# Performance work log

Hardware: AMD Instinct MI355X
Metric: run time of the kernel (lower is better)

Reference implementation:

```python
import jax, jax.numpy as jnp
import numpy as np

B, T, C, H = 2, 2048, 1024, 16
D = C // H  # head dim = 64

def setup_inputs() -> dict:
    key = jax.random.key(0)
    ks = jax.random.split(key, 5)
    s = 0.02
    return {
        "x": jax.random.normal(ks[0], (B, T, C), dtype=jnp.float32),
        "Wqkv": jax.random.normal(ks[1], (C, 3 * C), dtype=jnp.float32) * s,
        "bqkv": jnp.zeros((3 * C,), dtype=jnp.float32),
        "Wproj": jax.random.normal(ks[2], (C, C), dtype=jnp.float32) * s,
        "bproj": jnp.zeros((C,), dtype=jnp.float32),
    }

def reference(x, Wqkv, bqkv, Wproj, bproj):
    b, t, c = x.shape
    qkv = x @ Wqkv + bqkv                       # [B,T,3C]
    q, k, v = jnp.split(qkv, 3, axis=-1)
    # [B,T,C] -> [B,H,T,D]
    q = q.reshape(b, t, H, D).transpose(0, 2, 1, 3)
    k = k.reshape(b, t, H, D).transpose(0, 2, 1, 3)
    v = v.reshape(b, t, H, D).transpose(0, 2, 1, 3)
    scale = 1.0 / np.sqrt(D).astype(np.float32)
    attn = jnp.einsum('bhqd,bhkd->bhqk', q, k) * scale  # [B,H,T,T]
    causal = jnp.tril(jnp.ones((t, t), dtype=bool))
    attn = jnp.where(causal, attn, jnp.float32(-jnp.inf))
    attn = jax.nn.softmax(attn, axis=-1)
    y = jnp.einsum('bhqk,bhkd->bhqd', attn, v)          # [B,H,T,D]
    y = y.transpose(0, 2, 1, 3).reshape(b, t, c)        # [B,T,C]
    return y @ Wproj + bproj
```

## Files before the change

kernel.cpp:

```cpp
#include <hip/hip_runtime.h>
#include <stdint.h>

#define B_ 2
#define T_ 2048
#define C_ 1024
#define H_ 16
#define D_ 64
#define M_ (B_*T_)
#define BHTD_ (B_*H_*T_*D_)

typedef __bf16 bf16x8 __attribute__((ext_vector_type(8)));
typedef __bf16 bf16x4 __attribute__((ext_vector_type(4)));
typedef float f32x4 __attribute__((ext_vector_type(4)));

static __device__ __forceinline__ unsigned short f32_bf16(float f) {
    unsigned int u = __float_as_uint(f);
    u += 0x7FFFu + ((u >> 16) & 1u);
    return (unsigned short)(u >> 16);
}

__global__ void cast_kernel(const float* __restrict__ in, unsigned short* __restrict__ out, int n) {
    int i = (blockIdx.x * 256 + threadIdx.x) * 4;
    if (i >= n) return;
    float4 f = *(const float4*)(in + i);
    ushort4 o;
    o.x = f32_bf16(f.x); o.y = f32_bf16(f.y); o.z = f32_bf16(f.z); o.w = f32_bf16(f.w);
    *(ushort4*)(out + i) = o;
}

__global__ void transpose_cast_kernel(const float* __restrict__ W, unsigned short* __restrict__ Wt,
                                      int K, int N) {
    __shared__ float tile[32][33];
    int n0 = blockIdx.x * 32, k0 = blockIdx.y * 32;
    int tx = threadIdx.x, ty = threadIdx.y;
    #pragma unroll
    for (int j = 0; j < 32; j += 8)
        tile[ty + j][tx] = W[(size_t)(k0 + ty + j) * N + n0 + tx];
    __syncthreads();
    #pragma unroll
    for (int j = 0; j < 32; j += 8)
        Wt[(size_t)(n0 + ty + j) * K + k0 + tx] = f32_bf16(tile[tx][ty + j]);
}

template<int EPI>
__global__ __launch_bounds__(256) void gemm_bt(
    const unsigned short* __restrict__ A,
    const unsigned short* __restrict__ Bt,
    const float* __restrict__ bias,
    unsigned short* __restrict__ out_bf16,
    float* __restrict__ out_f32,
    int M, int N, int K)
{
    __shared__ unsigned short As[2][128 * 32];
    __shared__ unsigned short Bs[2][128 * 32];
    int tid = threadIdx.x;
    int lane = tid & 63, wid = tid >> 6;
    int fr = lane & 15, fg = lane >> 4;
    int row0 = blockIdx.x * 128, col0 = blockIdx.y * 128;
    int wm = (wid >> 1) * 64, wn = (wid & 1) * 64;

    f32x4 acc[4][4];
    #pragma unroll
    for (int i = 0; i < 4; ++i)
        #pragma unroll
        for (int j = 0; j < 4; ++j)
            acc[i][j] = (f32x4){0.f, 0.f, 0.f, 0.f};

    const int srw = lane >> 2;
    const int scl = (lane & 3) * 8;
    const int c0 = wid * 2, c1 = wid * 2 + 1;

    auto stage = [&](int buf, int k0) {
        __builtin_amdgcn_global_load_lds(
            (const __attribute__((address_space(1))) void*)(A + (size_t)(row0 + c0 * 16 + srw) * K + k0 + scl),
            (__attribute__((address_space(3))) void*)(As[buf] + c0 * 512), 16, 0, 0);
        __builtin_amdgcn_global_load_lds(
            (const __attribute__((address_space(1))) void*)(A + (size_t)(row0 + c1 * 16 + srw) * K + k0 + scl),
            (__attribute__((address_space(3))) void*)(As[buf] + c1 * 512), 16, 0, 0);
        __builtin_amdgcn_global_load_lds(
            (const __attribute__((address_space(1))) void*)(Bt + (size_t)(col0 + c0 * 16 + srw) * K + k0 + scl),
            (__attribute__((address_space(3))) void*)(Bs[buf] + c0 * 512), 16, 0, 0);
        __builtin_amdgcn_global_load_lds(
            (const __attribute__((address_space(1))) void*)(Bt + (size_t)(col0 + c1 * 16 + srw) * K + k0 + scl),
            (__attribute__((address_space(3))) void*)(Bs[buf] + c1 * 512), 16, 0, 0);
    };

    stage(0, 0);
    __syncthreads();

    int cur = 0;
    for (int k0 = 0; k0 < K; k0 += 32) {
        if (k0 + 32 < K) stage(cur ^ 1, k0 + 32);

        bf16x8 af[4], bfr[4];
        #pragma unroll
        for (int i = 0; i < 4; ++i) {
            af[i]  = *(const bf16x8*)(As[cur] + (wm + i * 16 + fr) * 32 + fg * 8);
            bfr[i] = *(const bf16x8*)(Bs[cur] + (wn + i * 16 + fr) * 32 + fg * 8);
        }
        #pragma unroll
        for (int mi = 0; mi < 4; ++mi)
            #pragma unroll
            for (int ni = 0; ni < 4; ++ni)
                acc[mi][ni] = __builtin_amdgcn_mfma_f32_16x16x32_bf16(af[mi], bfr[ni], acc[mi][ni], 0, 0, 0);

        __syncthreads();
        cur ^= 1;
    }

    #pragma unroll
    for (int mi = 0; mi < 4; ++mi) {
        int rowb = row0 + wm + mi * 16 + fg * 4;
        #pragma unroll
        for (int ni = 0; ni < 4; ++ni) {
            int col = col0 + wn + ni * 16 + fr;
            float bv = bias[col];
            #pragma unroll
            for (int r = 0; r < 4; ++r) {
                float v = acc[mi][ni][r] + bv;
                int rr = rowb + r;
                if (EPI == 0) {
                    int part = col >> 10, c = col & 1023;
                    int h = c >> 6, d = c & 63;
                    int b = rr >> 11, t = rr & 2047;
                    if (part == 0) v *= 0.18033688011112042f;
                    size_t idx;
                    if (part == 2)
                        idx = (size_t)2 * BHTD_ + ((size_t)(b * H_ + h) * D_ + d) * T_ + t;
                    else
                        idx = (size_t)part * BHTD_ + ((size_t)(b * H_ + h) * T_ + t) * D_ + d;
                    out_bf16[idx] = f32_bf16(v);
                } else {
                    out_f32[(size_t)rr * N + col] = v;
                }
            }
        }
    }
}

__global__ __launch_bounds__(256) void attn_kernel(
    const unsigned short* __restrict__ qg,
    const unsigned short* __restrict__ kg,
    const unsigned short* __restrict__ vtg,
    unsigned short* __restrict__ y)
{
    const int id = blockIdx.x;
    const int xcd = id & 7, loc = id >> 3;
    const int bh = xcd * 4 + (loc & 3);
    const int iq = loc >> 2;
    const int chlo = iq, chhi = 31 - iq;
    const int b = bh >> 4, h = bh & 15;
    const int tid = threadIdx.x, wid = tid >> 6, lane = tid & 63;
    const int fr = lane & 15, fg = lane >> 4;

    const unsigned short* qp = qg + (size_t)bh * (T_ * D_);
    const unsigned short* kp = kg + (size_t)bh * (T_ * D_);
    const unsigned short* vp = vtg + (size_t)bh * (D_ * T_);

    __shared__ __align__(16) char Ks[2][64 * 128];
    __shared__ __align__(16) char Vs[2][64 * 128];
    __shared__ __align__(16) char Ps[4][32 * 128];
    char* Pw = Ps[wid];

    const int rhi = chhi * 64 + wid * 16;
    const int rlo = chlo * 64 + wid * 16;

    const int srow = tid >> 3;
    const int scb  = (tid & 7) * 16;
    const int sws  = scb ^ ((srow & 7) << 4);

    bf16x8 qhi[2], qlo[2];
    #pragma unroll
    for (int kd = 0; kd < 2; ++kd) {
        qhi[kd] = *(const bf16x8*)(qp + (size_t)(rhi + fr) * D_ + kd * 32 + fg * 8);
        qlo[kd] = *(const bf16x8*)(qp + (size_t)(rlo + fr) * D_ + kd * 32 + fg * 8);
    }

    f32x4 oHi[4], oLo[4];
    float lHi = 0.f, lLo = 0.f;
    #pragma unroll
    for (int n = 0; n < 4; ++n) {
        oHi[n] = (f32x4){0.f, 0.f, 0.f, 0.f};
        oLo[n] = (f32x4){0.f, 0.f, 0.f, 0.f};
    }

    const int ntk  = chhi + 1;
    const int ntlo = chlo + 1;

    {
        uint4 k0 = *(const uint4*)(kp + (size_t)srow        * D_ + (scb >> 1));
        uint4 k1 = *(const uint4*)(kp + (size_t)(srow + 32) * D_ + (scb >> 1));
        uint4 v0 = *(const uint4*)(vp + (size_t)srow        * T_ + (scb >> 1));
        uint4 v1 = *(const uint4*)(vp + (size_t)(srow + 32) * T_ + (scb >> 1));
        *(uint4*)(Ks[0] + srow * 128 + sws)        = k0;
        *(uint4*)(Ks[0] + (srow + 32) * 128 + sws) = k1;
        *(uint4*)(Vs[0] + srow * 128 + sws)        = v0;
        *(uint4*)(Vs[0] + (srow + 32) * 128 + sws) = v1;
    }
    __syncthreads();

    int cur = 0;
    for (int t = 0; t < ntk; ++t) {
        const int kv0 = t * 64;
        const int kv1 = (t + 1 < ntk) ? kv0 + 64 : kv0;

        uint4 pk0 = *(const uint4*)(kp + (size_t)(kv1 + srow)      * D_ + (scb >> 1));
        uint4 pk1 = *(const uint4*)(kp + (size_t)(kv1 + srow + 32) * D_ + (scb >> 1));
        uint4 pv0 = *(const uint4*)(vp + (size_t)srow        * T_ + kv1 + (scb >> 1));
        uint4 pv1 = *(const uint4*)(vp + (size_t)(srow + 32) * T_ + kv1 + (scb >> 1));

        const char* Kb = Ks[cur];
        const char* Vb = Vs[cur];
        const unsigned lsw = (unsigned)((fr & 7) << 4);
        const bool lo_act = (t < ntlo);

        f32x4 sh[4], sl[4];
        #pragma unroll
        for (int n = 0; n < 4; ++n) {
            sh[n] = (f32x4){0.f, 0.f, 0.f, 0.f};
            sl[n] = (f32x4){0.f, 0.f, 0.f, 0.f};
        }
        #pragma unroll
        for (int kd = 0; kd < 2; ++kd)
            #pragma unroll
            for (int n = 0; n < 4; ++n) {
                bf16x8 kf = *(const bf16x8*)(Kb + (n * 16 + fr) * 128 +
                                             (((unsigned)(kd * 64 + fg * 16)) ^ lsw));
                sh[n] = __builtin_amdgcn_mfma_f32_16x16x32_bf16(kf, qhi[kd], sh[n], 0, 0, 0);
                if (lo_act)
                    sl[n] = __builtin_amdgcn_mfma_f32_16x16x32_bf16(kf, qlo[kd], sl[n], 0, 0, 0);
            }

        bf16x8 vf[4][2];
        #pragma unroll
        for (int nd = 0; nd < 4; ++nd)
            #pragma unroll
            for (int kk = 0; kk < 2; ++kk)
                vf[nd][kk] = *(const bf16x8*)(Vb + (nd * 16 + fr) * 128 +
                                              (((unsigned)(kk * 64 + fg * 16)) ^ lsw));

        {
            const bool masked = (t == chhi);
            const int qrow = rhi + fr;
            const unsigned prow = (unsigned)fr * 128;
            #pragma unroll
            for (int n = 0; n < 4; ++n) {
                float x0 = sh[n][0], x1 = sh[n][1], x2 = sh[n][2], x3 = sh[n][3];
                if (masked) {
                    const int kvb = kv0 + n * 16 + fg * 4;
                    if (kvb     > qrow) x0 = -1e30f;
                    if (kvb + 1 > qrow) x1 = -1e30f;
                    if (kvb + 2 > qrow) x2 = -1e30f;
                    if (kvb + 3 > qrow) x3 = -1e30f;
                }
                const float p0 = exp2f(x0), p1 = exp2f(x1);
                const float p2 = exp2f(x2), p3 = exp2f(x3);
                lHi += (p0 + p1) + (p2 + p3);
                bf16x4 pk4 = {(__bf16)p0, (__bf16)p1, (__bf16)p2, (__bf16)p3};
                *(uint2*)(Pw + ((prow + (unsigned)(n * 32 + fg * 8)) ^ lsw)) =
                    __builtin_bit_cast(uint2, pk4);
            }
        }
        {
            const unsigned prow = (unsigned)fr * 128;
            #pragma unroll
            for (int kk = 0; kk < 2; ++kk) {
                bf16x8 pb = *(const bf16x8*)(Pw + ((prow + (unsigned)(kk * 64 + fg * 16)) ^ lsw));
                #pragma unroll
                for (int nd = 0; nd < 4; ++nd)
                    oHi[nd] = __builtin_amdgcn_mfma_f32_16x16x32_bf16(vf[nd][kk], pb, oHi[nd], 0, 0, 0);
            }
        }
        if (lo_act) {
            const bool masked = (t == chlo);
            const int qrow = rlo + fr;
            const unsigned prow = (unsigned)(16 + fr) * 128;
            #pragma unroll
            for (int n = 0; n < 4; ++n) {
                float x0 = sl[n][0], x1 = sl[n][1], x2 = sl[n][2], x3 = sl[n][3];
                if (masked) {
                    const int kvb = kv0 + n * 16 + fg * 4;
                    if (kvb     > qrow) x0 = -1e30f;
                    if (kvb + 1 > qrow) x1 = -1e30f;
                    if (kvb + 2 > qrow) x2 = -1e30f;
                    if (kvb + 3 > qrow) x3 = -1e30f;
                }
                const float p0 = exp2f(x0), p1 = exp2f(x1);
                const float p2 = exp2f(x2), p3 = exp2f(x3);
                lLo += (p0 + p1) + (p2 + p3);
                bf16x4 pk4 = {(__bf16)p0, (__bf16)p1, (__bf16)p2, (__bf16)p3};
                *(uint2*)(Pw + ((prow + (unsigned)(n * 32 + fg * 8)) ^ lsw)) =
                    __builtin_bit_cast(uint2, pk4);
            }
            const unsigned prow2 = (unsigned)(16 + fr) * 128;
            #pragma unroll
            for (int kk = 0; kk < 2; ++kk) {
                bf16x8 pb = *(const bf16x8*)(Pw + ((prow2 + (unsigned)(kk * 64 + fg * 16)) ^ lsw));
                #pragma unroll
                for (int nd = 0; nd < 4; ++nd)
                    oLo[nd] = __builtin_amdgcn_mfma_f32_16x16x32_bf16(vf[nd][kk], pb, oLo[nd], 0, 0, 0);
            }
        }

        {
            char* Kn = Ks[cur ^ 1];
            char* Vn = Vs[cur ^ 1];
            *(uint4*)(Kn + srow * 128 + sws)        = pk0;
            *(uint4*)(Kn + (srow + 32) * 128 + sws) = pk1;
            *(uint4*)(Vn + srow * 128 + sws)        = pv0;
            *(uint4*)(Vn + (srow + 32) * 128 + sws) = pv1;
        }
        __syncthreads();
        cur ^= 1;
    }

    #pragma unroll
    for (int s = 0; s < 2; ++s) {
        float rs = s ? lLo : lHi;
        rs += __shfl_xor(rs, 16);
        rs += __shfl_xor(rs, 32);
        const float inv = 1.f / rs;
        const int trow = (s ? rlo : rhi) + fr;
        f32x4* oT = s ? oLo : oHi;
        #pragma unroll
        for (int nd = 0; nd < 4; ++nd) {
            bf16x4 ov = {(__bf16)(oT[nd][0] * inv), (__bf16)(oT[nd][1] * inv),
                         (__bf16)(oT[nd][2] * inv), (__bf16)(oT[nd][3] * inv)};
            *(uint2*)(y + ((size_t)b * T_ + trow) * C_ + h * 64 + nd * 16 + fg * 4) =
                __builtin_bit_cast(uint2, ov);
        }
    }
}

extern "C" void kernel_launch(void* const* d_in, const int* in_sizes, int n_in,
                              void* d_out, int out_size, void* d_ws, size_t ws_size,
                              hipStream_t stream) {
    const float* x     = (const float*)d_in[0];
    const float* Wqkv  = (const float*)d_in[1];
    const float* bqkv  = (const float*)d_in[2];
    const float* Wproj = (const float*)d_in[3];
    const float* bproj = (const float*)d_in[4];
    float* out = (float*)d_out;

    char* ws = (char*)d_ws;
    unsigned short* x_bf    = (unsigned short*)(ws);
    unsigned short* wqkv_t  = (unsigned short*)(ws + 8388608);
    unsigned short* wproj_t = (unsigned short*)(ws + 14680064);
    unsigned short* qkv     = (unsigned short*)(ws + 16777216);
    unsigned short* ybuf    = (unsigned short*)(ws + 41943040);

    cast_kernel<<<(M_ * C_) / 4 / 256, 256, 0, stream>>>(x, x_bf, M_ * C_);
    transpose_cast_kernel<<<dim3(3072 / 32, 1024 / 32), dim3(32, 8), 0, stream>>>(Wqkv, wqkv_t, 1024, 3072);
    transpose_cast_kernel<<<dim3(1024 / 32, 1024 / 32), dim3(32, 8), 0, stream>>>(Wproj, wproj_t, 1024, 1024);

    gemm_bt<0><<<dim3(M_ / 128, 3072 / 128), 256, 0, stream>>>(
        x_bf, wqkv_t, bqkv, qkv, nullptr, M_, 3072, 1024);

    attn_kernel<<<dim3(512), 256, 0, stream>>>(
        qkv, qkv + (size_t)BHTD_, qkv + 2 * (size_t)BHTD_, ybuf);

    gemm_bt<1><<<dim3(M_ / 128, 1024 / 128), 256, 0, stream>>>(
        ybuf, wproj_t, bproj, nullptr, out, M_, 1024, 1024);
}
```

Before: 126.5 us.

## Restructure attention to 32x32 MFMA tiles with direct-to-LDS loads and register P

Rewrites the attention kernel to use 32x32x16 MFMA with 128-thread blocks (two waves, 32 query rows each) over 1024 blocks. K/V tiles are staged with global_load_lds directly into LDS instead of going through registers. The P matrix stays in registers, repacked with permlane32_swap, instead of round-tripping through LDS. Causal load balancing moves from pairing hi/lo chunks within one block to ordering blocks by chunk. The intent is to cut LDS traffic and register staging and to raise MFMA efficiency, at the risk of lower per-block reuse and more blocks to schedule.

```diff
diff --git a/kernel.cpp b/kernel.cpp
--- a/kernel.cpp
+++ b/kernel.cpp
@@ -11,12 +11,19 @@
 
 typedef __bf16 bf16x8 __attribute__((ext_vector_type(8)));
 typedef __bf16 bf16x4 __attribute__((ext_vector_type(4)));
+typedef __bf16 bf16x2 __attribute__((ext_vector_type(2)));
 typedef float f32x4 __attribute__((ext_vector_type(4)));
+typedef float f32x16 __attribute__((ext_vector_type(16)));
 
 static __device__ __forceinline__ unsigned short f32_bf16(float f) {
     unsigned int u = __float_as_uint(f);
     u += 0x7FFFu + ((u >> 16) & 1u);
     return (unsigned short)(u >> 16);
+}
+
+static __device__ __forceinline__ int pack_bf16_2(float a, float b) {
+    bf16x2 v = {(__bf16)a, (__bf16)b};
+    return __builtin_bit_cast(int, v);
 }
 
 __global__ void cast_kernel(const float* __restrict__ in, unsigned short* __restrict__ out, int n) {
@@ -138,196 +145,191 @@
     }
 }
 
-__global__ __launch_bounds__(256) void attn_kernel(
+__global__ __launch_bounds__(128) void attn_kernel(
     const unsigned short* __restrict__ qg,
     const unsigned short* __restrict__ kg,
     const unsigned short* __restrict__ vtg,
     unsigned short* __restrict__ y)
 {
     const int id = blockIdx.x;
-    const int xcd = id & 7, loc = id >> 3;
-    const int bh = xcd * 4 + (loc & 3);
-    const int iq = loc >> 2;
-    const int chlo = iq, chhi = 31 - iq;
+    const int xcd = id & 7, j = id >> 3;
+    const int c = j & 31, g = j >> 5;
+    int chunk;
+    if      (g == 0) chunk = 31 - c;
+    else if (g == 1) chunk = c;
+    else if (g == 2) chunk = (15 - c) & 31;
+    else             chunk = (c + 16) & 31;
+    const int bh = xcd * 4 + (c >> 3);
     const int b = bh >> 4, h = bh & 15;
     const int tid = threadIdx.x, wid = tid >> 6, lane = tid & 63;
-    const int fr = lane & 15, fg = lane >> 4;
+    const int lq = lane & 31, hi = lane >> 5;
 
     const unsigned short* qp = qg + (size_t)bh * (T_ * D_);
-    const unsigned short* kp = kg + (size_t)bh * (T_ * D_);
-    const unsigned short* vp = vtg + (size_t)bh * (D_ * T_);
-
-    __shared__ __align__(16) char Ks[2][64 * 128];
-    __shared__ __align__(16) char Vs[2][64 * 128];
-    __shared__ __align__(16) char Ps[4][32 * 128];
-    char* Pw = Ps[wid];
-
-    const int rhi = chhi * 64 + wid * 16;
-    const int rlo = chlo * 64 + wid * 16;
-
-    const int srow = tid >> 3;
-    const int scb  = (tid & 7) * 16;
-    const int sws  = scb ^ ((srow & 7) << 4);
-
-    bf16x8 qhi[2], qlo[2];
-    #pragma unroll
-    for (int kd = 0; kd < 2; ++kd) {
-        qhi[kd] = *(const bf16x8*)(qp + (size_t)(rhi + fr) * D_ + kd * 32 + fg * 8);
-        qlo[kd] = *(const bf16x8*)(qp + (size_t)(rlo + fr) * D_ + kd * 32 + fg * 8);
-    }
-
-    f32x4 oHi[4], oLo[4];
-    float lHi = 0.f, lLo = 0.f;
-    #pragma unroll
-    for (int n = 0; n < 4; ++n) {
-        oHi[n] = (f32x4){0.f, 0.f, 0.f, 0.f};
-        oLo[n] = (f32x4){0.f, 0.f, 0.f, 0.f};
-    }
-
-    const int ntk  = chhi + 1;
-    const int ntlo = chlo + 1;
-
-    {
-        uint4 k0 = *(const uint4*)(kp + (size_t)srow        * D_ + (scb >> 1));
-        uint4 k1 = *(const uint4*)(kp + (size_t)(srow + 32) * D_ + (scb >> 1));
-        uint4 v0 = *(const uint4*)(vp + (size_t)srow        * T_ + (scb >> 1));
-        uint4 v1 = *(const uint4*)(vp + (size_t)(srow + 32) * T_ + (scb >> 1));
-        *(uint4*)(Ks[0] + srow * 128 + sws)        = k0;
-        *(uint4*)(Ks[0] + (srow + 32) * 128 + sws) = k1;
-        *(uint4*)(Vs[0] + srow * 128 + sws)        = v0;
-        *(uint4*)(Vs[0] + (srow + 32) * 128 + sws) = v1;
-    }
+    const char* kpB = (const char*)(kg + (size_t)bh * (T_ * D_));
+    const char* vpB = (const char*)(vtg + (size_t)bh * (D_ * T_));
+
+    __shared__ __align__(16) char Ks[2][8192];
+    __shared__ __align__(16) char Vs[2][8192];
+
+    const int r0 = chunk * 64 + wid * 32;
+    const int ntk = chunk + 1;
+
+    bf16x8 qf[4];
+    #pragma unroll
+    for (int ds = 0; ds < 4; ++ds)
+        qf[ds] = *(const bf16x8*)(qp + (size_t)(r0 + lq) * D_ + ds * 16 + hi * 8);
+
+    f32x16 oT0, oT1;
+    #pragma unroll
+    for (int e = 0; e < 16; ++e) { oT0[e] = 0.f; oT1[e] = 0.f; }
+    float lrun = 0.f;
+
+    const int srow8 = lane >> 3;
+    const int scol  = (lane & 7) * 16;
+    const int ssw   = srow8 << 4;
+
+    auto stage = [&](int buf, int kv0) {
+        #pragma unroll
+        for (int blk = 0; blk < 4; ++blk) {
+            const int rbase = wid * 32 + blk * 8;
+            __builtin_amdgcn_global_load_lds(
+                (const __attribute__((address_space(1))) void*)
+                    (kpB + (size_t)(kv0 + rbase + srow8) * 128 + (scol ^ ssw)),
+                (__attribute__((address_space(3))) void*)(Ks[buf] + rbase * 128), 16, 0, 0);
+            __builtin_amdgcn_global_load_lds(
+                (const __attribute__((address_space(1))) void*)
+                    (vpB + (size_t)(rbase + srow8) * 4096 + kv0 * 2 + (scol ^ ssw)),
+                (__attribute__((address_space(3))) void*)(Vs[buf] + rbase * 128), 16, 0, 0);
+        }
+    };
+
+    auto make_pb = [&](const f32x16& p, int g4a) -> bf16x8 {
+        int A0 = pack_bf16_2(p[g4a * 4 + 0], p[g4a * 4 + 1]);
+        int A1 = pack_bf16_2(p[g4a * 4 + 2], p[g4a * 4 + 3]);
+        int B0 = pack_bf16_2(p[g4a * 4 + 4], p[g4a * 4 + 5]);
+        int B1 = pack_bf16_2(p[g4a * 4 + 6], p[g4a * 4 + 7]);
+        auto ra = __builtin_amdgcn_permlane32_swap(A0, B0, false, false);
+        auto rb = __builtin_amdgcn_permlane32_swap(A1, B1, false, false);
+        int4 w;
+        w.x = ra[0]; w.y = rb[0]; w.z = ra[1]; w.w = rb[1];
+        return __builtin_bit_cast(bf16x8, w);
+    };
+
+    stage(0, 0);
     __syncthreads();
 
+    const int lsw = (lq & 7) << 4;
     int cur = 0;
     for (int t = 0; t < ntk; ++t) {
         const int kv0 = t * 64;
-        const int kv1 = (t + 1 < ntk) ? kv0 + 64 : kv0;
-
-        uint4 pk0 = *(const uint4*)(kp + (size_t)(kv1 + srow)      * D_ + (scb >> 1));
-        uint4 pk1 = *(const uint4*)(kp + (size_t)(kv1 + srow + 32) * D_ + (scb >> 1));
-        uint4 pv0 = *(const uint4*)(vp + (size_t)srow        * T_ + kv1 + (scb >> 1));
-        uint4 pv1 = *(const uint4*)(vp + (size_t)(srow + 32) * T_ + kv1 + (scb >> 1));
+        if (t + 1 < ntk) stage(cur ^ 1, kv0 + 64);
 
         const char* Kb = Ks[cur];
         const char* Vb = Vs[cur];
-        const unsigned lsw = (unsigned)((fr & 7) << 4);
-        const bool lo_act = (t < ntlo);
-
-        f32x4 sh[4], sl[4];
-        #pragma unroll
-        for (int n = 0; n < 4; ++n) {
-            sh[n] = (f32x4){0.f, 0.f, 0.f, 0.f};
-            sl[n] = (f32x4){0.f, 0.f, 0.f, 0.f};
-        }
-        #pragma unroll
-        for (int kd = 0; kd < 2; ++kd)
-            #pragma unroll
-            for (int n = 0; n < 4; ++n) {
-                bf16x8 kf = *(const bf16x8*)(Kb + (n * 16 + fr) * 128 +
-                                             (((unsigned)(kd * 64 + fg * 16)) ^ lsw));
-                sh[n] = __builtin_amdgcn_mfma_f32_16x16x32_bf16(kf, qhi[kd], sh[n], 0, 0, 0);
-                if (lo_act)
-                    sl[n] = __builtin_amdgcn_mfma_f32_16x16x32_bf16(kf, qlo[kd], sl[n], 0, 0, 0);
+        const bool diag = (t == chunk);
+        const bool do_n1 = !(diag && wid == 0);
+
+        f32x16 s0, s1;
+        #pragma unroll
+        for (int e = 0; e < 16; ++e) { s0[e] = 0.f; s1[e] = 0.f; }
+        #pragma unroll
+        for (int ds = 0; ds < 4; ++ds) {
+            bf16x8 kf = *(const bf16x8*)(Kb + lq * 128 + ((ds * 32 + hi * 16) ^ lsw));
+            s0 = __builtin_amdgcn_mfma_f32_32x32x16_bf16(kf, qf[ds], s0, 0, 0, 0);
+        }
+        if (do_n1) {
+            #pragma unroll
+            for (int ds = 0; ds < 4; ++ds) {
+                bf16x8 kf = *(const bf16x8*)(Kb + (32 + lq) * 128 + ((ds * 32 + hi * 16) ^ lsw));
+                s1 = __builtin_amdgcn_mfma_f32_32x32x16_bf16(kf, qf[ds], s1, 0, 0, 0);
             }
-
-        bf16x8 vf[4][2];
-        #pragma unroll
-        for (int nd = 0; nd < 4; ++nd)
-            #pragma unroll
-            for (int kk = 0; kk < 2; ++kk)
-                vf[nd][kk] = *(const bf16x8*)(Vb + (nd * 16 + fr) * 128 +
-                                              (((unsigned)(kk * 64 + fg * 16)) ^ lsw));
-
+        }
+
+        bf16x8 vf[2][4];
+        #pragma unroll
+        for (int dd = 0; dd < 2; ++dd)
+            #pragma unroll
+            for (int st = 0; st < 2; ++st)
+                vf[dd][st] = *(const bf16x8*)(Vb + (dd * 32 + lq) * 128 +
+                                              ((st * 32 + hi * 16) ^ lsw));
+        if (do_n1) {
+            #pragma unroll
+            for (int dd = 0; dd < 2; ++dd)
+                #pragma unroll
+                for (int st = 2; st < 4; ++st)
+                    vf[dd][st] = *(const bf16x8*)(Vb + (dd * 32 + lq) * 128 +
+                                                  ((st * 32 + hi * 16) ^ lsw));
+        }
+
+        const int qrow = r0 + lq;
+        if (diag && wid == 0) {
+            #pragma unroll
+            for (int e = 0; e < 16; ++e) {
+                const int kvl = (e & 3) + ((e >> 2) << 3) + hi * 4;
+                s0[e] = exp2f((kv0 + kvl <= qrow) ? s0[e] : -1e30f);
+            }
+        } else {
+            #pragma unroll
+            for (int e = 0; e < 16; ++e) s0[e] = exp2f(s0[e]);
+        }
         {
-            const bool masked = (t == chhi);
-            const int qrow = rhi + fr;
-            const unsigned prow = (unsigned)fr * 128;
-            #pragma unroll
-            for (int n = 0; n < 4; ++n) {
-                float x0 = sh[n][0], x1 = sh[n][1], x2 = sh[n][2], x3 = sh[n][3];
-                if (masked) {
-                    const int kvb = kv0 + n * 16 + fg * 4;
-                    if (kvb     > qrow) x0 = -1e30f;
-                    if (kvb + 1 > qrow) x1 = -1e30f;
-                    if (kvb + 2 > qrow) x2 = -1e30f;
-                    if (kvb + 3 > qrow) x3 = -1e30f;
+            float a0 = (s0[0] + s0[1]) + (s0[2] + s0[3]);
+            float a1 = (s0[4] + s0[5]) + (s0[6] + s0[7]);
+            float a2 = (s0[8] + s0[9]) + (s0[10] + s0[11]);
+            float a3 = (s0[12] + s0[13]) + (s0[14] + s0[15]);
+            lrun += (a0 + a1) + (a2 + a3);
+        }
+        if (do_n1) {
+            if (diag) {
+                #pragma unroll
+                for (int e = 0; e < 16; ++e) {
+                    const int kvl = 32 + (e & 3) + ((e >> 2) << 3) + hi * 4;
+                    s1[e] = exp2f((kv0 + kvl <= qrow) ? s1[e] : -1e30f);
                 }
-                const float p0 = exp2f(x0), p1 = exp2f(x1);
-                const float p2 = exp2f(x2), p3 = exp2f(x3);
-                lHi += (p0 + p1) + (p2 + p3);
-                bf16x4 pk4 = {(__bf16)p0, (__bf16)p1, (__bf16)p2, (__bf16)p3};
-                *(uint2*)(Pw + ((prow + (unsigned)(n * 32 + fg * 8)) ^ lsw)) =
-                    __builtin_bit_cast(uint2, pk4);
+            } else {
+                #pragma unroll
+                for (int e = 0; e < 16; ++e) s1[e] = exp2f(s1[e]);
             }
-        }
+            float a0 = (s1[0] + s1[1]) + (s1[2] + s1[3]);
+            float a1 = (s1[4] + s1[5]) + (s1[6] + s1[7]);
+            float a2 = (s1[8] + s1[9]) + (s1[10] + s1[11]);
+            float a3 = (s1[12] + s1[13]) + (s1[14] + s1[15]);
+            lrun += (a0 + a1) + (a2 + a3);
+        }
+
         {
-            const unsigned prow = (unsigned)fr * 128;
-            #pragma unroll
-            for (int kk = 0; kk < 2; ++kk) {
-                bf16x8 pb = *(const bf16x8*)(Pw + ((prow + (unsigned)(kk * 64 + fg * 16)) ^ lsw));
-                #pragma unroll
-                for (int nd = 0; nd < 4; ++nd)
-                    oHi[nd] = __builtin_amdgcn_mfma_f32_16x16x32_bf16(vf[nd][kk], pb, oHi[nd], 0, 0, 0);
-            }
-        }
-        if (lo_act) {
-            const bool masked = (t == chlo);
-            const int qrow = rlo + fr;
-            const unsigned prow = (unsigned)(16 + fr) * 128;
-            #pragma unroll
-            for (int n = 0; n < 4; ++n) {
-                float x0 = sl[n][0], x1 = sl[n][1], x2 = sl[n][2], x3 = sl[n][3];
-                if (masked) {
-                    const int kvb = kv0 + n * 16 + fg * 4;
-                    if (kvb     > qrow) x0 = -1e30f;
-                    if (kvb + 1 > qrow) x1 = -1e30f;
-                    if (kvb + 2 > qrow) x2 = -1e30f;
-                    if (kvb + 3 > qrow) x3 = -1e30f;
-                }
-                const float p0 = exp2f(x0), p1 = exp2f(x1);
-                const float p2 = exp2f(x2), p3 = exp2f(x3);
-                lLo += (p0 + p1) + (p2 + p3);
-                bf16x4 pk4 = {(__bf16)p0, (__bf16)p1, (__bf16)p2, (__bf16)p3};
-                *(uint2*)(Pw + ((prow + (unsigned)(n * 32 + fg * 8)) ^ lsw)) =
-                    __builtin_bit_cast(uint2, pk4);
-            }
-            const unsigned prow2 = (unsigned)(16 + fr) * 128;
-            #pragma unroll
-            for (int kk = 0; kk < 2; ++kk) {
-                bf16x8 pb = *(const bf16x8*)(Pw + ((prow2 + (unsigned)(kk * 64 + fg * 16)) ^ lsw));
-                #pragma unroll
-                for (int nd = 0; nd < 4; ++nd)
-                    oLo[nd] = __builtin_amdgcn_mfma_f32_16x16x32_bf16(vf[nd][kk], pb, oLo[nd], 0, 0, 0);
-            }
-        }
-
-        {
-            char* Kn = Ks[cur ^ 1];
-            char* Vn = Vs[cur ^ 1];
-            *(uint4*)(Kn + srow * 128 + sws)        = pk0;
-            *(uint4*)(Kn + (srow + 32) * 128 + sws) = pk1;
-            *(uint4*)(Vn + srow * 128 + sws)        = pv0;
-            *(uint4*)(Vn + (srow + 32) * 128 + sws) = pv1;
-        }
+            bf16x8 pb = make_pb(s0, 0);
+            oT0 = __builtin_amdgcn_mfma_f32_32x32x16_bf16(vf[0][0], pb, oT0, 0, 0, 0);
+            oT1 = __builtin_amdgcn_mfma_f32_32x32x16_bf16(vf[1][0], pb, oT1, 0, 0, 0);
+            pb = make_pb(s0, 2);
+            oT0 = __builtin_amdgcn_mfma_f32_32x32x16_bf16(vf[0][1], pb, oT0, 0, 0, 0);
+            oT1 = __builtin_amdgcn_mfma_f32_32x32x16_bf16(vf[1][1], pb, oT1, 0, 0, 0);
+        }
+        if (do_n1) {
+            bf16x8 pb = make_pb(s1, 0);
+            oT0 = __builtin_amdgcn_mfma_f32_32x32x16_bf16(vf[0][2], pb, oT0, 0, 0, 0);
+            oT1 = __builtin_amdgcn_mfma_f32_32x32x16_bf16(vf[1][2], pb, oT1, 0, 0, 0);
+            pb = make_pb(s1, 2);
+            oT0 = __builtin_amdgcn_mfma_f32_32x32x16_bf16(vf[0][3], pb, oT0, 0, 0, 0);
+            oT1 = __builtin_amdgcn_mfma_f32_32x32x16_bf16(vf[1][3], pb, oT1, 0, 0, 0);
+        }
+
         __syncthreads();
         cur ^= 1;
     }
 
-    #pragma unroll
-    for (int s = 0; s < 2; ++s) {
-        float rs = s ? lLo : lHi;
-        rs += __shfl_xor(rs, 16);
-        rs += __shfl_xor(rs, 32);
-        const float inv = 1.f / rs;
-        const int trow = (s ? rlo : rhi) + fr;
-        f32x4* oT = s ? oLo : oHi;
-        #pragma unroll
-        for (int nd = 0; nd < 4; ++nd) {
-            bf16x4 ov = {(__bf16)(oT[nd][0] * inv), (__bf16)(oT[nd][1] * inv),
-                         (__bf16)(oT[nd][2] * inv), (__bf16)(oT[nd][3] * inv)};
-            *(uint2*)(y + ((size_t)b * T_ + trow) * C_ + h * 64 + nd * 16 + fg * 4) =
-                __builtin_bit_cast(uint2, ov);
+    const float ls = lrun + __shfl_xor(lrun, 32);
+    const float inv = 1.f / ls;
+    const int trow = r0 + lq;
+    unsigned short* yrow = y + ((size_t)b * T_ + trow) * C_ + h * 64;
+    #pragma unroll
+    for (int dd = 0; dd < 2; ++dd) {
+        const f32x16& o = dd ? oT1 : oT0;
+        #pragma unroll
+        for (int g4 = 0; g4 < 4; ++g4) {
+            bf16x4 ov = {(__bf16)(o[g4 * 4 + 0] * inv), (__bf16)(o[g4 * 4 + 1] * inv),
+                         (__bf16)(o[g4 * 4 + 2] * inv), (__bf16)(o[g4 * 4 + 3] * inv)};
+            *(uint2*)(yrow + dd * 32 + g4 * 8 + hi * 4) = __builtin_bit_cast(uint2, ov);
         }
     }
 }
@@ -356,7 +358,7 @@
     gemm_bt<0><<<dim3(M_ / 128, 3072 / 128), 256, 0, stream>>>(
         x_bf, wqkv_t, bqkv, qkv, nullptr, M_, 3072, 1024);
 
-    attn_kernel<<<dim3(512), 256, 0, stream>>>(
+    attn_kernel<<<dim3(1024), 128, 0, stream>>>(
         qkv, qkv + (size_t)BHTD_, qkv + 2 * (size_t)BHTD_, ybuf);
 
     gemm_bt<1><<<dim3(M_ / 128, 1024 / 128), 256, 0, stream>>>(
```

After: 134.2 us. +6.0%, slower.
